# Performance work log

Hardware: AMD Instinct MI355X
Metric: run time of the kernel (lower is better)

The kernel has to match this reference:

```python
import jax, jax.numpy as jnp
import numpy as np

HIDDEN = 2048
NUM_HEADS = 8
NUM_KV_HEADS = 1
HEAD_DIM = 256
ROPE_THETA = 10000.0
T = 2048  # num tokens (single causal prefill sequence)
Q_SIZE = NUM_HEADS * HEAD_DIM        # 2048
KV_SIZE = NUM_KV_HEADS * HEAD_DIM    # 256


def _apply_rope(x, positions):
    # x: [T, n_heads, head_dim], neox style (rotate halves)
    half = HEAD_DIM // 2
    inv_freq = 1.0 / (ROPE_THETA ** (jnp.arange(half, dtype=jnp.float32) * 2.0 / HEAD_DIM))
    ang = positions.astype(jnp.float32)[:, None] * inv_freq[None, :]   # [T, half]
    cos = jnp.cos(ang)[:, None, :]
    sin = jnp.sin(ang)[:, None, :]
    x1, x2 = jnp.split(x, 2, axis=-1)
    return jnp.concatenate([x1 * cos - x2 * sin, x2 * cos + x1 * sin], axis=-1)


def setup_inputs() -> dict:
    key = jax.random.key(0)
    k1, k2, k3 = jax.random.split(key, 3)
    hidden_states = jax.random.normal(k1, (T, HIDDEN), dtype=jnp.float32)
    Wqkv = jax.random.normal(k2, (Q_SIZE + 2 * KV_SIZE, HIDDEN), dtype=jnp.float32) * 0.02
    Wo = jax.random.normal(k3, (HIDDEN, Q_SIZE), dtype=jnp.float32) * 0.02
    positions = jnp.arange(T, dtype=jnp.int32)
    return {"positions": positions, "hidden_states": hidden_states, "Wqkv": Wqkv, "Wo": Wo}


def reference(positions, hidden_states, Wqkv, Wo):
    scaling = HEAD_DIM ** -0.5
    qkv = hidden_states @ Wqkv.T                                   # [T, Q+2KV]
    q = qkv[:, :Q_SIZE].reshape(T, NUM_HEADS, HEAD_DIM)
    k = qkv[:, Q_SIZE:Q_SIZE + KV_SIZE].reshape(T, NUM_KV_HEADS, HEAD_DIM)
    v = qkv[:, Q_SIZE + KV_SIZE:].reshape(T, NUM_KV_HEADS, HEAD_DIM)
    q = _apply_rope(q, positions)
    k = _apply_rope(k, positions)
    # GQA: group query heads over kv heads
    g = NUM_HEADS // NUM_KV_HEADS
    qg = q.reshape(T, NUM_KV_HEADS, g, HEAD_DIM)
    scores = jnp.einsum('qhgd,khd->hgqk', qg, k) * scaling         # [kv, g, T, T]
    causal = jnp.arange(T)[:, None] >= jnp.arange(T)[None, :]
    scores = jnp.where(causal[None, None], scores, jnp.finfo(scores.dtype).min)
    probs = jax.nn.softmax(scores, axis=-1)
    attn = jnp.einsum('hgqk,khd->qhgd', probs, v).reshape(T, Q_SIZE)
    return attn @ Wo.T
```

## Files before the change

kernel.cpp:

```cpp
#include <hip/hip_runtime.h>
#include <hip/hip_bf16.h>

typedef __bf16 bf16x8 __attribute__((ext_vector_type(8)));
typedef __bf16 bf16x4 __attribute__((ext_vector_type(4)));
typedef float floatx4 __attribute__((ext_vector_type(4)));

__device__ __forceinline__ float fast_exp2(float x) {
    return __builtin_amdgcn_exp2f(x);
}

__device__ __forceinline__ void lds_barrier() {
    asm volatile("s_waitcnt lgkmcnt(0)\n\ts_barrier" ::: "memory");
}

__global__ __launch_bounds__(256) void cast_all(const float* __restrict__ hid,
                                                const float* __restrict__ wqkv,
                                                const float* __restrict__ wo,
                                                __bf16* __restrict__ Ah,
                                                __bf16* __restrict__ Wqkvh,
                                                __bf16* __restrict__ Woh) {
    const int n1 = 1048576, n2 = 1310720;
    int i = blockIdx.x * 256 + threadIdx.x;
    const float* in;
    __bf16* out;
    int j;
    if (i < n1) { in = hid; out = Ah; j = i; }
    else if (i < n1 + n2) { in = wqkv; out = Wqkvh; j = i - n1; }
    else { in = wo; out = Woh; j = i - n1 - n2; }
    float4 v = ((const float4*)in)[j];
    bf16x4 o;
    o[0] = (__bf16)v.x; o[1] = (__bf16)v.y; o[2] = (__bf16)v.z; o[3] = (__bf16)v.w;
    ((bf16x4*)out)[j] = o;
}

template<typename OutT>
__global__ __launch_bounds__(256) void gemm_bt(const __bf16* __restrict__ A,
                                               const __bf16* __restrict__ B,
                                               OutT* __restrict__ C,
                                               int M, int N, int K) {
    __shared__ __attribute__((aligned(16))) __bf16 As[128 * 64];
    __shared__ __attribute__((aligned(16))) __bf16 Bs[128 * 64];

    int tid = threadIdx.x, lane = tid & 63, w = tid >> 6;
    int wm = (w >> 1) * 64, wn = (w & 1) * 64;
    int bm0 = blockIdx.x * 128, bn0 = blockIdx.y * 128;
    int r = lane & 15, q4 = lane >> 4;
    int rr = lane >> 2, qq = lane & 3;

    const __bf16* Agp[4];
    const __bf16* Bgp[4];
    __bf16* Asd[4];
    __bf16* Bsd[4];
#pragma unroll
    for (int j = 0; j < 4; j++) {
        int c = w * 4 + j;
        int kk = c >> 3, g = c & 7;
        Agp[j] = A + (size_t)(bm0 + g * 16 + rr) * K + kk * 32 + qq * 8;
        Bgp[j] = B + (size_t)(bn0 + g * 16 + rr) * K + kk * 32 + qq * 8;
        Asd[j] = &As[c * 512 + lane * 8];
        Bsd[j] = &Bs[c * 512 + lane * 8];
    }

    floatx4 acc[4][4];
#pragma unroll
    for (int i = 0; i < 4; i++)
#pragma unroll
        for (int j = 0; j < 4; j++) acc[i][j] = (floatx4)0.f;

    bf16x8 ar[4], br[4];
#pragma unroll
    for (int j = 0; j < 4; j++) {
        ar[j] = *(const bf16x8*)Agp[j];
        br[j] = *(const bf16x8*)Bgp[j];
    }

    for (int k0 = 0; k0 < K; k0 += 64) {
        lds_barrier();
#pragma unroll
        for (int j = 0; j < 4; j++) {
            *(bf16x8*)Asd[j] = ar[j];
            *(bf16x8*)Bsd[j] = br[j];
        }
        if (k0 + 64 < K) {
#pragma unroll
            for (int j = 0; j < 4; j++) {
                ar[j] = *(const bf16x8*)(Agp[j] + k0 + 64);
                br[j] = *(const bf16x8*)(Bgp[j] + k0 + 64);
            }
        }
        lds_barrier();

#pragma unroll
        for (int kk = 0; kk < 2; kk++) {
            bf16x8 a[4], b[4];
#pragma unroll
            for (int mt = 0; mt < 4; mt++)
                a[mt] = *(const bf16x8*)&As[(kk * 8 + (wm >> 4) + mt) * 512 + r * 32 + q4 * 8];
#pragma unroll
            for (int nt = 0; nt < 4; nt++)
                b[nt] = *(const bf16x8*)&Bs[(kk * 8 + (wn >> 4) + nt) * 512 + r * 32 + q4 * 8];
#pragma unroll
            for (int mt = 0; mt < 4; mt++)
#pragma unroll
                for (int nt = 0; nt < 4; nt++)
                    acc[mt][nt] = __builtin_amdgcn_mfma_f32_16x16x32_bf16(a[mt], b[nt], acc[mt][nt], 0, 0, 0);
        }
    }

#pragma unroll
    for (int mt = 0; mt < 4; mt++)
#pragma unroll
        for (int nt = 0; nt < 4; nt++) {
            int row = bm0 + wm + mt * 16 + q4 * 4;
            int col = bn0 + wn + nt * 16 + r;
#pragma unroll
            for (int i = 0; i < 4; i++)
                C[(size_t)(row + i) * N + col] = (OutT)acc[mt][nt][i];
        }
}

__global__ __launch_bounds__(256) void rope_vtrans(const __bf16* __restrict__ qkv,
                                                   const int* __restrict__ positions,
                                                   __bf16* __restrict__ Qo,
                                                   __bf16* __restrict__ Ko,
                                                   __bf16* __restrict__ Vt) {
    __shared__ float tile[32][33];
    int b = blockIdx.x;
    if (b < 9216) {
        int idx = b * 256 + threadIdx.x;
        int i = idx & 127;
        int th = idx >> 7;
        int head = th % 9;
        int t = th / 9;
        float invf = expf(-(float)i * 0.07195578415606394f);
        float ang = (float)positions[t] * invf;
        float s = sinf(ang), c = cosf(ang);
        size_t off = (size_t)t * 2560 + (head < 8 ? head * 256 : 2048);
        float x1 = (float)qkv[off + i];
        float x2 = (float)qkv[off + i + 128];
        if (head < 8) {
            const float qs = 0.09016844f;
            __bf16* dst = Qo + (size_t)t * 2048 + head * 256;
            dst[i]       = (__bf16)((x1 * c - x2 * s) * qs);
            dst[i + 128] = (__bf16)((x2 * c + x1 * s) * qs);
        } else {
            __bf16* dst = Ko + (size_t)t * 256;
            dst[i]       = (__bf16)(x1 * c - x2 * s);
            dst[i + 128] = (__bf16)(x2 * c + x1 * s);
        }
    } else {
        int bb = b - 9216;
        int bt = bb & 63;
        int bc = bb >> 6;
        int tx = threadIdx.x & 31;
        int ty0 = threadIdx.x >> 5;
#pragma unroll
        for (int ty = ty0; ty < 32; ty += 8)
            tile[ty][tx] = (float)qkv[(size_t)(bt * 32 + ty) * 2560 + 2304 + bc * 32 + tx];
        __syncthreads();
#pragma unroll
        for (int ty = ty0; ty < 32; ty += 8)
            Vt[(size_t)(bc * 32 + ty) * 2048 + bt * 32 + tx] = (__bf16)tile[tx][ty];
    }
}

__global__ __launch_bounds__(256) void attn_kernel(const __bf16* __restrict__ Q,
                                                   const __bf16* __restrict__ Kg,
                                                   const __bf16* __restrict__ Vt,
                                                   __bf16* __restrict__ Opart,
                                                   float2* __restrict__ Ml) {
    __shared__ __attribute__((aligned(16))) __bf16 Ks[32 * 264];
    __shared__ __attribute__((aligned(16))) __bf16 Vs[256 * 40];
    __shared__ __attribute__((aligned(16))) __bf16 Ps[4][16][40];

    int hg = blockIdx.x;
    int rs = 407 - (int)blockIdx.y;
    int k, base;
    if (rs < 24)       { k = 1; base = 0; }
    else if (rs < 72)  { k = 2; base = 24; }
    else if (rs < 144) { k = 3; base = 72; }
    else if (rs < 240) { k = 4; base = 144; }
    else if (rs < 360) { k = 5; base = 240; }
    else               { k = 6; base = 360; }
    int idx = rs - base;
    int s = idx % k;
    int g = (k - 1) * 24 + idx / k;
    int slot = base + idx - s;

    int start = s * 384;
    int end = g * 16 + 16;
    if (end > start + 384) end = start + 384;
    int ntiles = (end - start + 31) >> 5;

    int tid = threadIdx.x, lane = tid & 63, w = tid >> 6;
    int r = lane & 15, q4 = lane >> 4;
    int h = hg * 4 + w;

    int krow = w * 8 + (lane & 7);
    int kcol = (lane >> 3) * 32;
    int vrow = w * 64 + lane;
    __bf16* kd = &Ks[krow * 264 + kcol];
    __bf16* vd = &Vs[vrow * 40];

    bf16x8 qf[8];
    {
        const __bf16* qrow = Q + (size_t)(g * 16 + r) * 2048 + h * 256 + q4 * 8;
#pragma unroll
        for (int ks = 0; ks < 8; ks++) qf[ks] = *(const bf16x8*)(qrow + ks * 32);
    }

    bf16x8 ones;
#pragma unroll
    for (int i = 0; i < 8; i++) ones[i] = (__bf16)1.0f;

    floatx4 acc[16];
#pragma unroll
    for (int i = 0; i < 16; i++) acc[i] = (floatx4)0.f;
    floatx4 acc_l = (floatx4)0.f;

    bf16x8 kr[4], vr[4];
    {
        const __bf16* kp = Kg + (size_t)(start + krow) * 256 + kcol;
        const __bf16* vp = Vt + (size_t)vrow * 2048 + start;
#pragma unroll
        for (int j = 0; j < 4; j++) {
            kr[j] = *(const bf16x8*)(kp + j * 8);
            vr[j] = *(const bf16x8*)(vp + j * 8);
        }
    }

    for (int t = 0; t < ntiles; t++) {
        int kt0 = start + t * 32;
        lds_barrier();
#pragma unroll
        for (int j = 0; j < 4; j++) {
            *(bf16x8*)(kd + j * 8) = kr[j];
            *(bf16x8*)(vd + j * 8) = vr[j];
        }
        if (t + 1 < ntiles) {
            const __bf16* kp = Kg + (size_t)(kt0 + 32 + krow) * 256 + kcol;
            const __bf16* vp = Vt + (size_t)vrow * 2048 + kt0 + 32;
#pragma unroll
            for (int j = 0; j < 4; j++) {
                kr[j] = *(const bf16x8*)(kp + j * 8);
                vr[j] = *(const bf16x8*)(vp + j * 8);
            }
        }
        lds_barrier();

        floatx4 sc[2];
        sc[0] = (floatx4)0.f; sc[1] = (floatx4)0.f;
#pragma unroll
        for (int ks = 0; ks < 8; ks++) {
#pragma unroll
            for (int nt = 0; nt < 2; nt++) {
                bf16x8 kf = *(const bf16x8*)&Ks[(nt * 16 + r) * 264 + ks * 32 + q4 * 8];
                sc[nt] = __builtin_amdgcn_mfma_f32_16x16x32_bf16(qf[ks], kf, sc[nt], 0, 0, 0);
            }
        }
        if (kt0 + 31 > g * 16) {
            int qbase = g * 16 + q4 * 4;
#pragma unroll
            for (int nt = 0; nt < 2; nt++) {
                int kpos = kt0 + nt * 16 + r;
#pragma unroll
                for (int i = 0; i < 4; i++)
                    if (kpos > qbase + i) sc[nt][i] = -3e38f;
            }
        }

#pragma unroll
        for (int nt = 0; nt < 2; nt++)
#pragma unroll
            for (int i = 0; i < 4; i++)
                Ps[w][q4 * 4 + i][(nt * 16 + r) ^ (q4 << 3)] = (__bf16)fast_exp2(sc[nt][i]);
        __builtin_amdgcn_wave_barrier();
        bf16x8 pf = *(const bf16x8*)&Ps[w][r][(q4 * 8) ^ ((r >> 2) << 3)];
        __builtin_amdgcn_wave_barrier();

#pragma unroll
        for (int n16 = 0; n16 < 16; n16++) {
            bf16x8 vf = *(const bf16x8*)&Vs[(n16 * 16 + r) * 40 + q4 * 8];
            acc[n16] = __builtin_amdgcn_mfma_f32_16x16x32_bf16(pf, vf, acc[n16], 0, 0, 0);
        }
        acc_l = __builtin_amdgcn_mfma_f32_16x16x32_bf16(pf, ones, acc_l, 0, 0, 0);
    }

    size_t base_row = (size_t)(slot + s) * 128 + hg * 64 + w * 16;
#pragma unroll
    for (int n16 = 0; n16 < 16; n16++)
#pragma unroll
        for (int i = 0; i < 4; i++)
            Opart[(base_row + q4 * 4 + i) * 256 + n16 * 16 + r] = (__bf16)acc[n16][i];
    if (r == 0) {
#pragma unroll
        for (int i = 0; i < 4; i++)
            Ml[base_row + q4 * 4 + i] = make_float2(0.f, acc_l[i]);
    }
}

__global__ __launch_bounds__(256) void combine_kernel(const __bf16* __restrict__ Opart,
                                                      const float2* __restrict__ Ml,
                                                      __bf16* __restrict__ attnb) {
    int wid = blockIdx.x * 4 + (threadIdx.x >> 6);
    int lane = threadIdx.x & 63;
    int t = wid >> 3, h = wid & 7;
    int g = t >> 4, row = t & 15;
    int hg = h >> 2, w = h & 3;
    int nsp = g / 24 + 1;
    int full = g / 24, rem = g % 24;
    int fg = 12 * full * (full + 1) + rem * (full + 1);

    float ms[6], ls[6];
    size_t rbase[6];
    float M = -3e38f;
    for (int s = 0; s < nsp; s++) {
        rbase[s] = (size_t)(fg + s) * 128 + hg * 64 + w * 16 + row;
        float2 ml = Ml[rbase[s]];
        ms[s] = ml.x; ls[s] = ml.y;
        M = fmaxf(M, ml.x);
    }
    float L = 0.f;
    float o[4] = {0.f, 0.f, 0.f, 0.f};
    for (int s = 0; s < nsp; s++) {
        float wsc = fast_exp2(ms[s] - M);
        L += ls[s] * wsc;
        bf16x4 v = *(const bf16x4*)&Opart[rbase[s] * 256 + lane * 4];
#pragma unroll
        for (int j = 0; j < 4; j++) o[j] += wsc * (float)v[j];
    }
    float inv = 1.f / L;
    bf16x4 ov;
#pragma unroll
    for (int j = 0; j < 4; j++) ov[j] = (__bf16)(o[j] * inv);
    *(bf16x4*)&attnb[(size_t)t * 2048 + h * 256 + lane * 4] = ov;
}

extern "C" void kernel_launch(void* const* d_in, const int* in_sizes, int n_in,
                              void* d_out, int out_size, void* d_ws, size_t ws_size,
                              hipStream_t stream) {
    const int* positions = (const int*)d_in[0];
    const float* hidden  = (const float*)d_in[1];
    const float* Wqkv    = (const float*)d_in[2];
    const float* Wo      = (const float*)d_in[3];
    float* out = (float*)d_out;

    char* ws = (char*)d_ws;
    const size_t MB = 1024 * 1024;
    __bf16* Ah    = (__bf16*)(ws + 0 * MB);
    __bf16* Woh   = (__bf16*)(ws + 8 * MB);
    __bf16* Qb    = (__bf16*)(ws + 16 * MB);
    __bf16* Kb    = (__bf16*)(ws + 24 * MB);
    __bf16* Vtb   = (__bf16*)(ws + 25 * MB);
    __bf16* Wqkvh = (__bf16*)(ws + 26 * MB);
    __bf16* qkvb  = (__bf16*)(ws + 36 * MB);
    __bf16* Opart = (__bf16*)(ws + 26 * MB);
    float2* Ml    = (float2*)(ws + 52 * MB);
    __bf16* attnb = Ah;

    cast_all<<<13312, 256, 0, stream>>>(hidden, Wqkv, Wo, Ah, Wqkvh, Woh);

    gemm_bt<__bf16><<<dim3(16, 20), 256, 0, stream>>>(Ah, Wqkvh, qkvb, 2048, 2560, 2048);

    rope_vtrans<<<9728, 256, 0, stream>>>(qkvb, positions, Qb, Kb, Vtb);

    attn_kernel<<<dim3(2, 408), 256, 0, stream>>>(Qb, Kb, Vtb, Opart, Ml);
    combine_kernel<<<4096, 256, 0, stream>>>(Opart, Ml, attnb);

    gemm_bt<float><<<dim3(16, 16), 256, 0, stream>>>(attnb, Woh, out, 2048, 2048, 2048);
}
```

Baseline: 241.4 us.

## Fuse fp32-to-bf16 casts into GEMM loads and retile V for attention

Removes the separate cast kernel. The GEMMs now load fp32 inputs straight from global memory and convert them to bf16 before the shared-memory store, which avoids writing and re-reading the bf16 copies. In exchange the GEMMs read twice the bytes per element and hold more prefetch registers. The transposed V is also stored in 32-token tile blocks so the attention kernel's V staging uses contiguous loads and conflict-free LDS reads without padding.

New measurement: 255.9 us. 6.0% more time.

```diff
diff --git a/kernel.cpp b/kernel.cpp
--- a/kernel.cpp
+++ b/kernel.cpp
@@ -13,29 +13,27 @@
     asm volatile("s_waitcnt lgkmcnt(0)\n\ts_barrier" ::: "memory");
 }
 
-__global__ __launch_bounds__(256) void cast_all(const float* __restrict__ hid,
-                                                const float* __restrict__ wqkv,
-                                                const float* __restrict__ wo,
-                                                __bf16* __restrict__ Ah,
-                                                __bf16* __restrict__ Wqkvh,
-                                                __bf16* __restrict__ Woh) {
-    const int n1 = 1048576, n2 = 1310720;
-    int i = blockIdx.x * 256 + threadIdx.x;
-    const float* in;
-    __bf16* out;
-    int j;
-    if (i < n1) { in = hid; out = Ah; j = i; }
-    else if (i < n1 + n2) { in = wqkv; out = Wqkvh; j = i - n1; }
-    else { in = wo; out = Woh; j = i - n1 - n2; }
-    float4 v = ((const float4*)in)[j];
-    bf16x4 o;
-    o[0] = (__bf16)v.x; o[1] = (__bf16)v.y; o[2] = (__bf16)v.z; o[3] = (__bf16)v.w;
-    ((bf16x4*)out)[j] = o;
-}
-
-template<typename OutT>
-__global__ __launch_bounds__(256) void gemm_bt(const __bf16* __restrict__ A,
-                                               const __bf16* __restrict__ B,
+struct f32x8 { float4 lo, hi; };
+template<typename T> struct Raw;
+template<> struct Raw<__bf16> { using type = bf16x8; };
+template<> struct Raw<float>  { using type = f32x8; };
+
+__device__ __forceinline__ void load_raw(const __bf16* p, bf16x8& d) { d = *(const bf16x8*)p; }
+__device__ __forceinline__ void load_raw(const float* p, f32x8& d) {
+    d.lo = *(const float4*)p;
+    d.hi = *(const float4*)(p + 4);
+}
+__device__ __forceinline__ bf16x8 to_bf16(const bf16x8& v) { return v; }
+__device__ __forceinline__ bf16x8 to_bf16(const f32x8& v) {
+    bf16x8 o;
+    o[0] = (__bf16)v.lo.x; o[1] = (__bf16)v.lo.y; o[2] = (__bf16)v.lo.z; o[3] = (__bf16)v.lo.w;
+    o[4] = (__bf16)v.hi.x; o[5] = (__bf16)v.hi.y; o[6] = (__bf16)v.hi.z; o[7] = (__bf16)v.hi.w;
+    return o;
+}
+
+template<typename AT, typename BT, typename OutT>
+__global__ __launch_bounds__(256) void gemm_bt(const AT* __restrict__ A,
+                                               const BT* __restrict__ B,
                                                OutT* __restrict__ C,
                                                int M, int N, int K) {
     __shared__ __attribute__((aligned(16))) __bf16 As[128 * 64];
@@ -47,8 +45,8 @@
     int r = lane & 15, q4 = lane >> 4;
     int rr = lane >> 2, qq = lane & 3;
 
-    const __bf16* Agp[4];
-    const __bf16* Bgp[4];
+    const AT* Agp[4];
+    const BT* Bgp[4];
     __bf16* Asd[4];
     __bf16* Bsd[4];
 #pragma unroll
@@ -67,25 +65,26 @@
 #pragma unroll
         for (int j = 0; j < 4; j++) acc[i][j] = (floatx4)0.f;
 
-    bf16x8 ar[4], br[4];
+    typename Raw<AT>::type ar[4];
+    typename Raw<BT>::type br[4];
 #pragma unroll
     for (int j = 0; j < 4; j++) {
-        ar[j] = *(const bf16x8*)Agp[j];
-        br[j] = *(const bf16x8*)Bgp[j];
+        load_raw(Agp[j], ar[j]);
+        load_raw(Bgp[j], br[j]);
     }
 
     for (int k0 = 0; k0 < K; k0 += 64) {
         lds_barrier();
 #pragma unroll
         for (int j = 0; j < 4; j++) {
-            *(bf16x8*)Asd[j] = ar[j];
-            *(bf16x8*)Bsd[j] = br[j];
+            *(bf16x8*)Asd[j] = to_bf16(ar[j]);
+            *(bf16x8*)Bsd[j] = to_bf16(br[j]);
         }
         if (k0 + 64 < K) {
 #pragma unroll
             for (int j = 0; j < 4; j++) {
-                ar[j] = *(const bf16x8*)(Agp[j] + k0 + 64);
-                br[j] = *(const bf16x8*)(Bgp[j] + k0 + 64);
+                load_raw(Agp[j] + k0 + 64, ar[j]);
+                load_raw(Bgp[j] + k0 + 64, br[j]);
             }
         }
         lds_barrier();
@@ -160,7 +159,7 @@
         __syncthreads();
 #pragma unroll
         for (int ty = ty0; ty < 32; ty += 8)
-            Vt[(size_t)(bc * 32 + ty) * 2048 + bt * 32 + tx] = (__bf16)tile[tx][ty];
+            Vt[(size_t)bt * 8192 + (bc * 32 + ty) * 32 + tx] = (__bf16)tile[tx][ty];
     }
 }
 
@@ -170,7 +169,7 @@
                                                    __bf16* __restrict__ Opart,
                                                    float2* __restrict__ Ml) {
     __shared__ __attribute__((aligned(16))) __bf16 Ks[32 * 264];
-    __shared__ __attribute__((aligned(16))) __bf16 Vs[256 * 40];
+    __shared__ __attribute__((aligned(16))) __bf16 Vs[16 * 512];
     __shared__ __attribute__((aligned(16))) __bf16 Ps[4][16][40];
 
     int hg = blockIdx.x;
@@ -198,9 +197,9 @@
 
     int krow = w * 8 + (lane & 7);
     int kcol = (lane >> 3) * 32;
-    int vrow = w * 64 + lane;
     __bf16* kd = &Ks[krow * 264 + kcol];
-    __bf16* vd = &Vs[vrow * 40];
+    __bf16* vd = &Vs[(tid >> 4) * 512 + (tid & 15) * 8];
+    const __bf16* vgp = Vt + (size_t)tid * 32;
 
     bf16x8 qf[8];
     {
@@ -221,7 +220,7 @@
     bf16x8 kr[4], vr[4];
     {
         const __bf16* kp = Kg + (size_t)(start + krow) * 256 + kcol;
-        const __bf16* vp = Vt + (size_t)vrow * 2048 + start;
+        const __bf16* vp = vgp + (size_t)(start >> 5) * 8192;
 #pragma unroll
         for (int j = 0; j < 4; j++) {
             kr[j] = *(const bf16x8*)(kp + j * 8);
@@ -235,11 +234,11 @@
 #pragma unroll
         for (int j = 0; j < 4; j++) {
             *(bf16x8*)(kd + j * 8) = kr[j];
-            *(bf16x8*)(vd + j * 8) = vr[j];
+            *(bf16x8*)(vd + j * 128) = vr[j];
         }
         if (t + 1 < ntiles) {
             const __bf16* kp = Kg + (size_t)(kt0 + 32 + krow) * 256 + kcol;
-            const __bf16* vp = Vt + (size_t)vrow * 2048 + kt0 + 32;
+            const __bf16* vp = vgp + (size_t)((kt0 + 32) >> 5) * 8192;
 #pragma unroll
             for (int j = 0; j < 4; j++) {
                 kr[j] = *(const bf16x8*)(kp + j * 8);
@@ -280,7 +279,7 @@
 
 #pragma unroll
         for (int n16 = 0; n16 < 16; n16++) {
-            bf16x8 vf = *(const bf16x8*)&Vs[(n16 * 16 + r) * 40 + q4 * 8];
+            bf16x8 vf = *(const bf16x8*)&Vs[n16 * 512 + lane * 8];
             acc[n16] = __builtin_amdgcn_mfma_f32_16x16x32_bf16(pf, vf, acc[n16], 0, 0, 0);
         }
         acc_l = __builtin_amdgcn_mfma_f32_16x16x32_bf16(pf, ones, acc_l, 0, 0, 0);
@@ -347,25 +346,22 @@
 
     char* ws = (char*)d_ws;
     const size_t MB = 1024 * 1024;
-    __bf16* Ah    = (__bf16*)(ws + 0 * MB);
-    __bf16* Woh   = (__bf16*)(ws + 8 * MB);
-    __bf16* Qb    = (__bf16*)(ws + 16 * MB);
-    __bf16* Kb    = (__bf16*)(ws + 24 * MB);
-    __bf16* Vtb   = (__bf16*)(ws + 25 * MB);
-    __bf16* Wqkvh = (__bf16*)(ws + 26 * MB);
-    __bf16* qkvb  = (__bf16*)(ws + 36 * MB);
-    __bf16* Opart = (__bf16*)(ws + 26 * MB);
-    float2* Ml    = (float2*)(ws + 52 * MB);
-    __bf16* attnb = Ah;
-
-    cast_all<<<13312, 256, 0, stream>>>(hidden, Wqkv, Wo, Ah, Wqkvh, Woh);
-
-    gemm_bt<__bf16><<<dim3(16, 20), 256, 0, stream>>>(Ah, Wqkvh, qkvb, 2048, 2560, 2048);
+    __bf16* Qb    = (__bf16*)(ws + 0 * MB);
+    __bf16* Kb    = (__bf16*)(ws + 8 * MB);
+    __bf16* Vtb   = (__bf16*)(ws + 9 * MB);
+    __bf16* qkvb  = (__bf16*)(ws + 10 * MB);
+    __bf16* attnb = (__bf16*)(ws + 20 * MB);
+    __bf16* Opart = (__bf16*)(ws + 28 * MB);
+    float2* Ml    = (float2*)(ws + 54 * MB);
+
+    gemm_bt<float, float, __bf16><<<dim3(16, 20), 256, 0, stream>>>(hidden, Wqkv, qkvb,
+                                                                    2048, 2560, 2048);
 
     rope_vtrans<<<9728, 256, 0, stream>>>(qkvb, positions, Qb, Kb, Vtb);
 
     attn_kernel<<<dim3(2, 408), 256, 0, stream>>>(Qb, Kb, Vtb, Opart, Ml);
     combine_kernel<<<4096, 256, 0, stream>>>(Opart, Ml, attnb);
 
-    gemm_bt<float><<<dim3(16, 16), 256, 0, stream>>>(attnb, Woh, out, 2048, 2048, 2048);
-}
+    gemm_bt<__bf16, float, float><<<dim3(16, 16), 256, 0, stream>>>(attnb, Wo, out,
+                                                                    2048, 2048, 2048);
+}
```
